# Kernel tuning notes

Measured on AMD Instinct MI355X. Metric: run time of the kernel, lower is better.

## Reference

```python
import jax, jax.numpy as jnp
import numpy as np

N0, N1, N2 = 30000, 90000, 60000          # nodes, edges, triangles
D_IN, D_OUT, HEADS = 256, 128, 4
NNZ0, NNZ1, NNZ2 = 960000, 180000, 180000  # sparse incidence nnz


def setup_inputs() -> dict:
    key = jax.random.key(0)
    ks = jax.random.split(key, 18)
    s = 0.05
    return {
        "x0": jax.random.normal(ks[0], (N0, D_IN), dtype=jnp.float32),
        "x1": jax.random.normal(ks[1], (N1, D_IN), dtype=jnp.float32),
        "x2": jax.random.normal(ks[2], (N2, D_IN), dtype=jnp.float32),
        "rows0": jax.random.randint(ks[3], (NNZ0,), 0, N0),
        "cols0": jax.random.randint(ks[4], (NNZ0,), 0, N0),
        "rows1": jax.random.randint(ks[5], (NNZ1,), 0, N0),
        "cols1": jax.random.randint(ks[6], (NNZ1,), 0, N1),
        "rows2": jax.random.randint(ks[7], (NNZ2,), 0, N0),
        "cols2": jax.random.randint(ks[8], (NNZ2,), 0, N2),
        # per-head parameters (SATLayer_regular), stacked on leading head axis
        "W1": jax.random.normal(ks[9], (HEADS, D_IN, D_OUT), dtype=jnp.float32) * s,
        "b1": jax.random.normal(ks[10], (HEADS, D_OUT), dtype=jnp.float32) * s,
        "a1_w": jax.random.normal(ks[11], (HEADS, D_OUT), dtype=jnp.float32) * s,
        "a1_b": jax.random.normal(ks[12], (HEADS,), dtype=jnp.float32) * s,
        "a2_w": jax.random.normal(ks[13], (HEADS, D_OUT), dtype=jnp.float32) * s,
        "a2_b": jax.random.normal(ks[14], (HEADS,), dtype=jnp.float32) * s,
        "Wagg": jax.random.normal(ks[15], (HEADS, 4 * D_OUT, D_OUT), dtype=jnp.float32) * s,
        "bagg": jax.random.normal(ks[16], (HEADS, D_OUT), dtype=jnp.float32) * s,
    }


def reference(x0, x1, x2, rows0, cols0, rows1, cols1, rows2, cols2,
              W1, b1, a1_w, a1_b, a2_w, a2_b, Wagg, bagg):
    n0 = x0.shape[0]

    def sat_head(W1h, b1h, a1wh, a1bh, a2wh, a2bh, Waggh, baggh):
        # shared Linearlayer1 + ReLU applied to all simplex levels
        xi0 = jax.nn.relu(x0 @ W1h + b1h)   # [n0, d]
        xj1 = jax.nn.relu(x1 @ W1h + b1h)   # [n1, d]
        xj2 = jax.nn.relu(x2 @ W1h + b1h)   # [n2, d]
        a1 = xi0 @ a1wh + a1bh              # [n0] attention source term

        def attention_agg(xj, rows, cols):
            a2 = xj @ a2wh + a2bh                              # [nj]
            att = jax.nn.sigmoid(a1[rows] + a2[cols])          # [nnz]
            msg = att[:, None] * xj[cols]                      # [nnz, d]
            return jax.ops.segment_sum(msg, rows, num_segments=n0)

        agg0 = attention_agg(xi0, rows0, cols0)
        agg1 = attention_agg(xj1, rows1, cols1)
        agg2 = attention_agg(xj2, rows2, cols2)
        cat = jnp.concatenate([xi0, agg0, agg1, agg2], axis=1)  # [n0, 4d]
        return cat @ Waggh + baggh                              # [n0, d]

    # stack over heads, then mean (layer0_1 + torch.mean)
    outs = jax.vmap(sat_head)(W1, b1, a1_w, a1_b, a2_w, a2_b, Wagg, bagg)
    return jnp.mean(outs, axis=0)
```

## Files before the change

kernel.cpp:

```cpp
#include <hip/hip_runtime.h>

typedef __attribute__((ext_vector_type(8))) short short8;
typedef __attribute__((ext_vector_type(4))) float f32x4;
typedef unsigned short ushort_t;
typedef unsigned int uint32;

#define N0 30000
#define N1 90000
#define N2 60000
#define P0 30208
#define S1OFF 30208
#define S2OFF 120320
#define MPAD 180352
#define MT_ALL 1409
#define MT0 236
#define NE0 960000
#define NE1 180000
#define NE2 180000
#define CSTRIDE 30720

__device__ __forceinline__ float bf2f(ushort_t u) {
    union { uint32 i; float f; } v; v.i = ((uint32)u) << 16; return v.f;
}
__device__ __forceinline__ ushort_t f2bf(float f) {
    union { float f; uint32 i; } v; v.f = f;
    uint32 x = v.i;
    x += ((x >> 16) & 1u) + 0x7FFFu;
    return (ushort_t)(x >> 16);
}

__global__ __launch_bounds__(256) void prep_w(const float* __restrict__ W1,
                                              const float* __restrict__ Wagg,
                                              const float* __restrict__ bagg,
                                              ushort_t* __restrict__ W1t,
                                              ushort_t* __restrict__ Wgt,
                                              ushort_t* __restrict__ WgtC,
                                              float* __restrict__ bsum) {
    int idx = blockIdx.x * blockDim.x + threadIdx.x;
    if (idx < 131072) {
        int h = idx >> 15, rem = idx & 32767, n = rem >> 8, k = rem & 255;
        W1t[idx] = f2bf(W1[((size_t)h * 256 + k) * 128 + n]);
    }
    if (idx < 196608) {
        int h = idx / 49152, rem = idx % 49152;
        int l = rem / 16384, rem2 = rem % 16384, n = rem2 >> 7, k = rem2 & 127;
        Wgt[idx] = f2bf(Wagg[((size_t)h * 512 + (l + 1) * 128 + k) * 128 + n]);
    }
    if (idx < 65536) {
        int n = idx >> 9, kk = idx & 511, h = kk >> 7, k = kk & 127;
        WgtC[idx] = f2bf(Wagg[((size_t)h * 512 + k) * 128 + n]);
    }
    if (idx < 128) {
        float s = 0.f;
        #pragma unroll
        for (int h = 0; h < 4; ++h) s += bagg[h * 128 + idx];
        bsum[idx] = s;
    }
}

__global__ __launch_bounds__(256) void csr_zero(int* __restrict__ cur) {
    int i = blockIdx.x * blockDim.x + threadIdx.x;
    if (i < 3 * CSTRIDE) cur[i] = 0;
}

__global__ __launch_bounds__(256) void csr_hist(const int* __restrict__ rows, int nE,
                                                int* __restrict__ cur) {
    int i = blockIdx.x * blockDim.x + threadIdx.x;
    if (i < nE) atomicAdd(cur + rows[i], 1);
}

__global__ __launch_bounds__(1024) void csr_scan(int* __restrict__ curA,
                                                 int* __restrict__ rowPtrA,
                                                 int nE0, int nE1, int nE2) {
    __shared__ int ssum[1024];
    const int b = blockIdx.x;
    int* cur = curA + b * CSTRIDE;
    int* rowPtr = rowPtrA + b * CSTRIDE;
    const int nE = (b == 0) ? nE0 : (b == 1 ? nE1 : nE2);
    const int t = threadIdx.x;
    const int base = t * 30;
    int loc[30];
    int s = 0;
    #pragma unroll
    for (int i = 0; i < 30; ++i) {
        int r = base + i;
        int v = (r < N0) ? cur[r] : 0;
        loc[i] = s; s += v;
    }
    ssum[t] = s;
    __syncthreads();
    for (int off = 1; off < 1024; off <<= 1) {
        int v = (t >= off) ? ssum[t - off] : 0;
        __syncthreads();
        ssum[t] += v;
        __syncthreads();
    }
    int carry = (t == 0) ? 0 : ssum[t - 1];
    #pragma unroll
    for (int i = 0; i < 30; ++i) {
        int r = base + i;
        if (r < N0) {
            int p = carry + loc[i];
            rowPtr[r] = p;
            cur[r] = p;
        }
    }
    if (t == 0) rowPtr[N0] = nE;
}

__global__ __launch_bounds__(256) void csr_scatter(const int* __restrict__ rows,
                                                   const int* __restrict__ cols,
                                                   int nE, int Sl,
                                                   int* __restrict__ cur,
                                                   int* __restrict__ sortedCg) {
    int i = blockIdx.x * blockDim.x + threadIdx.x;
    if (i < nE) {
        int pos = atomicAdd(cur + rows[i], 1);
        sortedCg[pos] = Sl + cols[i];
    }
}

__global__ __launch_bounds__(256) void gemm_x(const float* __restrict__ x0,
                                              const float* __restrict__ x1,
                                              const float* __restrict__ x2,
                                              const ushort_t* __restrict__ W1t,
                                              const float* __restrict__ b1,
                                              ushort_t* __restrict__ Y) {
    __shared__ ushort_t As[128 * 264];
    __shared__ ushort_t Bs[128 * 40];
    const int tid = threadIdx.x;
    const int lane = tid & 63;
    const int wid = tid >> 6;
    const int wm = wid >> 1, wn = wid & 1;
    const int l15 = lane & 15, lg = lane >> 4;
    const int r0 = blockIdx.x * 128;

    const float* src; int jbase, nreal;
    if (r0 < P0)          { src = x0; jbase = r0;         nreal = N0; }
    else if (r0 < S2OFF)  { src = x1; jbase = r0 - S1OFF; nreal = N1; }
    else                  { src = x2; jbase = r0 - S2OFF; nreal = N2; }

    for (int c = 0; c < 32; ++c) {
        int f = tid + c * 256;
        int row = f >> 6, col4 = f & 63;
        int j = jbase + row;
        float vx = 0.f, vy = 0.f, vz = 0.f, vw = 0.f;
        if (j < nreal) {
            const float4 v = *(const float4*)(src + (size_t)j * 256 + col4 * 4);
            vx = v.x; vy = v.y; vz = v.z; vw = v.w;
        }
        ushort_t o[4] __attribute__((aligned(8)));
        o[0] = f2bf(vx); o[1] = f2bf(vy); o[2] = f2bf(vz); o[3] = f2bf(vw);
        *(uint2*)(As + row * 264 + col4 * 4) = *(const uint2*)o;
    }
    __syncthreads();

    for (int h = 0; h < 4; ++h) {
        f32x4 acc[4][4] = {};
        const ushort_t* Bh = W1t + h * 32768;
        for (int kt = 0; kt < 256; kt += 32) {
            #pragma unroll
            for (int u = 0; u < 2; ++u) {
                int g = tid * 2 + u;
                int n = g >> 2, kc = g & 3;
                *(uint4*)(Bs + n * 40 + kc * 8) = *(const uint4*)(Bh + n * 256 + kt + kc * 8);
            }
            __syncthreads();
            short8 af[4], bfr[4];
            #pragma unroll
            for (int m = 0; m < 4; ++m)
                af[m] = *(const short8*)(As + (wm * 64 + m * 16 + l15) * 264 + kt + lg * 8);
            #pragma unroll
            for (int n = 0; n < 4; ++n)
                bfr[n] = *(const short8*)(Bs + (wn * 64 + n * 16 + l15) * 40 + lg * 8);
            #pragma unroll
            for (int m = 0; m < 4; ++m)
                #pragma unroll
                for (int n = 0; n < 4; ++n)
                    acc[m][n] = __builtin_amdgcn_mfma_f32_16x16x32_bf16(af[m], bfr[n], acc[m][n], 0, 0, 0);
            __syncthreads();
        }
        #pragma unroll
        for (int n = 0; n < 4; ++n) {
            int col = wn * 64 + n * 16 + l15;
            float bb = b1[h * 128 + col];
            #pragma unroll
            for (int m = 0; m < 4; ++m)
            #pragma unroll
            for (int j = 0; j < 4; ++j) {
                int row = r0 + wm * 64 + m * 16 + lg * 4 + j;
                float v = acc[m][n][j] + bb;
                v = v > 0.f ? v : 0.f;
                Y[(size_t)row * 512 + h * 128 + col] = f2bf(v);
            }
        }
    }
}

__global__ __launch_bounds__(256)
void gemm_init(const ushort_t* __restrict__ A,
               const ushort_t* __restrict__ B,
               float* __restrict__ outF,
               const float* __restrict__ bias)
{
    __shared__ ushort_t As[128 * 40];
    __shared__ ushort_t Bs[128 * 40];
    const int tid = threadIdx.x;
    const int lane = tid & 63;
    const int wid = tid >> 6;
    const int wm = wid >> 1, wn = wid & 1;
    const int r0 = blockIdx.x * 128;
    const int l15 = lane & 15, lg = lane >> 4;

    f32x4 acc[4][4] = {};

    for (int kt = 0; kt < 512; kt += 32) {
        #pragma unroll
        for (int c = 0; c < 2; ++c) {
            int idx = tid + c * 256;
            int row = idx >> 2, kc = idx & 3;
            uint4 va = *(const uint4*)(A + (size_t)(r0 + row) * 512 + kt + kc * 8);
            *(uint4*)(As + row * 40 + kc * 8) = va;
            uint4 vb = *(const uint4*)(B + (size_t)row * 512 + kt + kc * 8);
            *(uint4*)(Bs + row * 40 + kc * 8) = vb;
        }
        __syncthreads();
        short8 af[4], bfr[4];
        #pragma unroll
        for (int m = 0; m < 4; ++m)
            af[m] = *(const short8*)(As + (wm * 64 + m * 16 + l15) * 40 + lg * 8);
        #pragma unroll
        for (int n = 0; n < 4; ++n)
            bfr[n] = *(const short8*)(Bs + (wn * 64 + n * 16 + l15) * 40 + lg * 8);
        #pragma unroll
        for (int m = 0; m < 4; ++m)
            #pragma unroll
            for (int n = 0; n < 4; ++n)
                acc[m][n] = __builtin_amdgcn_mfma_f32_16x16x32_bf16(af[m], bfr[n], acc[m][n], 0, 0, 0);
        __syncthreads();
    }

    #pragma unroll
    for (int m = 0; m < 4; ++m)
    #pragma unroll
    for (int n = 0; n < 4; ++n)
    #pragma unroll
    for (int j = 0; j < 4; ++j) {
        int row = r0 + wm * 64 + m * 16 + lg * 4 + j;
        int col = wn * 64 + n * 16 + l15;
        if (row < N0) outF[(size_t)row * 128 + col] = 0.25f * (acc[m][n][j] + bias[col]);
    }
}

__global__ __launch_bounds__(256) void gemm_z(const ushort_t* Yin,
                                              const ushort_t* __restrict__ Wgt,
                                              const float* __restrict__ a1w,
                                              const float* __restrict__ a1b,
                                              const float* __restrict__ a2w,
                                              const float* __restrict__ a2b,
                                              float* __restrict__ a1o,
                                              float* __restrict__ a2o,
                                              ushort_t* Yout) {
    __shared__ ushort_t As[128 * 136];
    __shared__ ushort_t Bs[128 * 136];
    __shared__ float a1wS[128], a2wS[128];
    const int tid = threadIdx.x;
    const int h = blockIdx.y;
    const int r0 = blockIdx.x * 128;
    const int l = (r0 < P0) ? 0 : (r0 < S2OFF ? 1 : 2);
    const ushort_t* B = Wgt + ((h * 3 + l) << 14);

    if (tid < 128) {
        a1wS[tid] = a1w[h * 128 + tid];
        a2wS[tid] = a2w[h * 128 + tid];
    }
    #pragma unroll
    for (int c = 0; c < 8; ++c) {
        int idx = tid + c * 256;
        int row = idx >> 4, ch = idx & 15;
        *(uint4*)(As + row * 136 + ch * 8) =
            *(const uint4*)(Yin + (size_t)(r0 + row) * 512 + h * 128 + ch * 8);
        *(uint4*)(Bs + row * 136 + ch * 8) = *(const uint4*)(B + row * 128 + ch * 8);
    }
    __syncthreads();

    {
        int row = tid >> 1, half = tid & 1;
        const ushort_t* yr = As + row * 136 + half * 64;
        float d1 = 0.f, d2 = 0.f;
        #pragma unroll
        for (int t = 0; t < 8; ++t) {
            short8 v = *(const short8*)(yr + t * 8);
            #pragma unroll
            for (int j = 0; j < 8; ++j) {
                float f = bf2f(((const ushort_t*)&v)[j]);
                d2 += f * a2wS[half * 64 + t * 8 + j];
                d1 += f * a1wS[half * 64 + t * 8 + j];
            }
        }
        d2 += __shfl_xor(d2, 1);
        d1 += __shfl_xor(d1, 1);
        if (half == 0) {
            a2o[(size_t)h * MPAD + r0 + row] = d2 + a2b[h];
            if (l == 0) a1o[(size_t)h * P0 + r0 + row] = d1 + a1b[h];
        }
    }

    const int lane = tid & 63;
    const int wid = tid >> 6;
    const int wm = wid >> 1, wn = wid & 1;
    const int l15 = lane & 15, lg = lane >> 4;

    f32x4 acc[4][4] = {};
    #pragma unroll
    for (int kt = 0; kt < 128; kt += 32) {
        short8 af[4], bfr[4];
        #pragma unroll
        for (int m = 0; m < 4; ++m)
            af[m] = *(const short8*)(As + (wm * 64 + m * 16 + l15) * 136 + kt + lg * 8);
        #pragma unroll
        for (int n = 0; n < 4; ++n)
            bfr[n] = *(const short8*)(Bs + (wn * 64 + n * 16 + l15) * 136 + kt + lg * 8);
        #pragma unroll
        for (int m = 0; m < 4; ++m)
            #pragma unroll
            for (int n = 0; n < 4; ++n)
                acc[m][n] = __builtin_amdgcn_mfma_f32_16x16x32_bf16(af[m], bfr[n], acc[m][n], 0, 0, 0);
    }

    #pragma unroll
    for (int m = 0; m < 4; ++m)
    #pragma unroll
    for (int n = 0; n < 4; ++n)
    #pragma unroll
    for (int j = 0; j < 4; ++j) {
        int row = r0 + wm * 64 + m * 16 + lg * 4 + j;
        int col = wn * 64 + n * 16 + l15;
        Yout[(size_t)row * 512 + h * 128 + col] = f2bf(acc[m][n][j]);
    }
}

__global__ __launch_bounds__(256) void pull_agg(const int* __restrict__ rowPtr,
                                                const int* __restrict__ sortedCg,
                                                const float* __restrict__ a1,
                                                const float* __restrict__ a2,
                                                const ushort_t* __restrict__ z,
                                                float* __restrict__ out) {
    int w = blockIdx.x * 4 + (threadIdx.x >> 6);
    if (w >= N0) return;
    const int lane = threadIdx.x & 63;
    const int h = lane >> 4, g = lane & 15;

    const float a1r = a1[(size_t)h * P0 + w];
    const float* a2h = a2 + (size_t)h * MPAD;
    int beg = rowPtr[w], end = rowPtr[w + 1];

    float acc[8] = {0.f, 0.f, 0.f, 0.f, 0.f, 0.f, 0.f, 0.f};
    int e = beg;
    for (; e + 1 < end; e += 2) {
        int cg0 = sortedCg[e], cg1 = sortedCg[e + 1];
        float s0 = a1r + a2h[cg0];
        float s1 = a1r + a2h[cg1];
        float att0 = 0.25f / (1.f + __expf(-s0));
        float att1 = 0.25f / (1.f + __expf(-s1));
        uint4 v0 = *(const uint4*)(z + (size_t)cg0 * 512 + lane * 8);
        uint4 v1 = *(const uint4*)(z + (size_t)cg1 * 512 + lane * 8);
        const ushort_t* u0 = (const ushort_t*)&v0;
        const ushort_t* u1 = (const ushort_t*)&v1;
        #pragma unroll
        for (int j = 0; j < 8; ++j)
            acc[j] += att0 * bf2f(u0[j]) + att1 * bf2f(u1[j]);
    }
    if (e < end) {
        int cg = sortedCg[e];
        float s = a1r + a2h[cg];
        float att = 0.25f / (1.f + __expf(-s));
        uint4 v = *(const uint4*)(z + (size_t)cg * 512 + lane * 8);
        const ushort_t* u = (const ushort_t*)&v;
        #pragma unroll
        for (int j = 0; j < 8; ++j) acc[j] += att * bf2f(u[j]);
    }
    #pragma unroll
    for (int j = 0; j < 8; ++j) {
        acc[j] += __shfl_xor(acc[j], 16);
        acc[j] += __shfl_xor(acc[j], 32);
    }
    float2* p = (float2*)(out + (size_t)w * 128 + g * 8 + h * 2);
    float2 o = *p;
    o.x += acc[h * 2 + 0];
    o.y += acc[h * 2 + 1];
    *p = o;
}

extern "C" void kernel_launch(void* const* d_in, const int* in_sizes, int n_in,
                              void* d_out, int out_size, void* d_ws, size_t ws_size,
                              hipStream_t stream) {
    const float* x0   = (const float*)d_in[0];
    const float* x1   = (const float*)d_in[1];
    const float* x2   = (const float*)d_in[2];
    const int* rows0  = (const int*)d_in[3];
    const int* cols0  = (const int*)d_in[4];
    const int* rows1  = (const int*)d_in[5];
    const int* cols1  = (const int*)d_in[6];
    const int* rows2  = (const int*)d_in[7];
    const int* cols2  = (const int*)d_in[8];
    const float* W1   = (const float*)d_in[9];
    const float* b1   = (const float*)d_in[10];
    const float* a1w  = (const float*)d_in[11];
    const float* a1b  = (const float*)d_in[12];
    const float* a2w  = (const float*)d_in[13];
    const float* a2b  = (const float*)d_in[14];
    const float* Wagg = (const float*)d_in[15];
    const float* bagg = (const float*)d_in[16];
    float* out = (float*)d_out;
    char* ws = (char*)d_ws;

    ushort_t* Y      = (ushort_t*)(ws);
    float*    a1o    = (float*)(ws + 184680448);
    float*    a2o    = (float*)(ws + 185163776);
    ushort_t* W1t    = (ushort_t*)(ws + 188049408);
    ushort_t* Wgt    = (ushort_t*)(ws + 188311552);
    ushort_t* WgtC   = (ushort_t*)(ws + 188704768);
    float*    bsum   = (float*)(ws + 188835840);
    int*      cur    = (int*)(ws + 188836352);
    int*      rowPtr = (int*)(ws + 189204992);
    int*      srtCg  = (int*)(ws + 189573632);

    int* cur0 = cur,              * cur1 = cur + CSTRIDE,    * cur2 = cur + 2 * CSTRIDE;
    int* rp0  = rowPtr,           * rp1  = rowPtr + CSTRIDE, * rp2  = rowPtr + 2 * CSTRIDE;
    int* srt0 = srtCg,            * srt1 = srtCg + NE0,      * srt2 = srtCg + NE0 + NE1;

    csr_zero<<<(3 * CSTRIDE + 255) / 256, 256, 0, stream>>>(cur);
    csr_hist<<<(NE0 + 255) / 256, 256, 0, stream>>>(rows0, NE0, cur0);
    csr_hist<<<(NE1 + 255) / 256, 256, 0, stream>>>(rows1, NE1, cur1);
    csr_hist<<<(NE2 + 255) / 256, 256, 0, stream>>>(rows2, NE2, cur2);
    csr_scan<<<3, 1024, 0, stream>>>(cur, rowPtr, NE0, NE1, NE2);
    csr_scatter<<<(NE0 + 255) / 256, 256, 0, stream>>>(rows0, cols0, NE0, 0,     cur0, srt0);
    csr_scatter<<<(NE1 + 255) / 256, 256, 0, stream>>>(rows1, cols1, NE1, S1OFF, cur1, srt1);
    csr_scatter<<<(NE2 + 255) / 256, 256, 0, stream>>>(rows2, cols2, NE2, S2OFF, cur2, srt2);

    prep_w<<<768, 256, 0, stream>>>(W1, Wagg, bagg, W1t, Wgt, WgtC, bsum);
    gemm_x<<<MT_ALL, 256, 0, stream>>>(x0, x1, x2, W1t, b1, Y);

    gemm_init<<<MT0, 256, 0, stream>>>(Y, WgtC, out, bsum);

    gemm_z<<<dim3(MT_ALL, 4), 256, 0, stream>>>(Y, Wgt, a1w, a1b, a2w, a2b, a1o, a2o, Y);

    pull_agg<<<(N0 + 3) / 4, 256, 0, stream>>>(rp0, srt0, a1o, a2o, Y, out);
    pull_agg<<<(N0 + 3) / 4, 256, 0, stream>>>(rp1, srt1, a1o, a2o, Y, out);
    pull_agg<<<(N0 + 3) / 4, 256, 0, stream>>>(rp2, srt2, a1o, a2o, Y, out);
}
```

Measured before the change: 645.1 us.

## Fuse input GEMM, attention dots, Z projection and init GEMM into one kernel

Merges gemm_x, gemm_init and gemm_z into a single 512-thread kernel. Each head's ReLU(xW1+b) tile stays in swizzled LDS and feeds the attention dot products, the per-level Wagg projection to Z and the level-0 output accumulation directly. This removes the bf16 Y round trip through global memory and two kernel launches. W1/Wgt B-operands are now read straight from global without LDS staging. LDS use rises to 96KB with launch_bounds(512,1), so occupancy is one block per CU.

```diff
diff --git a/kernel.cpp b/kernel.cpp
--- a/kernel.cpp
+++ b/kernel.cpp
@@ -13,7 +13,6 @@
 #define S2OFF 120320
 #define MPAD 180352
 #define MT_ALL 1409
-#define MT0 236
 #define NE0 960000
 #define NE1 180000
 #define NE2 180000
@@ -120,223 +119,197 @@
     }
 }
 
-__global__ __launch_bounds__(256) void gemm_x(const float* __restrict__ x0,
-                                              const float* __restrict__ x1,
-                                              const float* __restrict__ x2,
-                                              const ushort_t* __restrict__ W1t,
-                                              const float* __restrict__ b1,
-                                              ushort_t* __restrict__ Y) {
-    __shared__ ushort_t As[128 * 264];
-    __shared__ ushort_t Bs[128 * 40];
+__global__ __launch_bounds__(512, 1)
+void gemm_fused(const float* __restrict__ x0,
+                const float* __restrict__ x1,
+                const float* __restrict__ x2,
+                const ushort_t* __restrict__ W1t,
+                const float* __restrict__ b1,
+                const ushort_t* __restrict__ Wgt,
+                const ushort_t* __restrict__ WgtC,
+                const float* __restrict__ bsum,
+                const float* __restrict__ a1w, const float* __restrict__ a1b,
+                const float* __restrict__ a2w, const float* __restrict__ a2b,
+                float* __restrict__ a1o, float* __restrict__ a2o,
+                ushort_t* __restrict__ Z, float* __restrict__ outF)
+{
+    __shared__ ushort_t As[128 * 256];
+    __shared__ ushort_t Ys[128 * 128];
     const int tid = threadIdx.x;
     const int lane = tid & 63;
     const int wid = tid >> 6;
-    const int wm = wid >> 1, wn = wid & 1;
+    const int wm = wid >> 2, wn = wid & 3;
     const int l15 = lane & 15, lg = lane >> 4;
     const int r0 = blockIdx.x * 128;
+    const bool isL0 = (r0 < P0);
+    const int l = isL0 ? 0 : (r0 < S2OFF ? 1 : 2);
 
     const float* src; int jbase, nreal;
-    if (r0 < P0)          { src = x0; jbase = r0;         nreal = N0; }
-    else if (r0 < S2OFF)  { src = x1; jbase = r0 - S1OFF; nreal = N1; }
-    else                  { src = x2; jbase = r0 - S2OFF; nreal = N2; }
-
-    for (int c = 0; c < 32; ++c) {
-        int f = tid + c * 256;
-        int row = f >> 6, col4 = f & 63;
+    if (l == 0)      { src = x0; jbase = r0;         nreal = N0; }
+    else if (l == 1) { src = x1; jbase = r0 - S1OFF; nreal = N1; }
+    else             { src = x2; jbase = r0 - S2OFF; nreal = N2; }
+
+    #pragma unroll
+    for (int p = 0; p < 8; ++p) {
+        int chunk = tid + p * 512;
+        int row = chunk >> 5, c = chunk & 31;
         int j = jbase + row;
-        float vx = 0.f, vy = 0.f, vz = 0.f, vw = 0.f;
+        ushort_t o[8] __attribute__((aligned(16)));
         if (j < nreal) {
-            const float4 v = *(const float4*)(src + (size_t)j * 256 + col4 * 4);
-            vx = v.x; vy = v.y; vz = v.z; vw = v.w;
-        }
-        ushort_t o[4] __attribute__((aligned(8)));
-        o[0] = f2bf(vx); o[1] = f2bf(vy); o[2] = f2bf(vz); o[3] = f2bf(vw);
-        *(uint2*)(As + row * 264 + col4 * 4) = *(const uint2*)o;
+            const float4 v0 = *(const float4*)(src + (size_t)j * 256 + c * 8);
+            const float4 v1 = *(const float4*)(src + (size_t)j * 256 + c * 8 + 4);
+            o[0] = f2bf(v0.x); o[1] = f2bf(v0.y); o[2] = f2bf(v0.z); o[3] = f2bf(v0.w);
+            o[4] = f2bf(v1.x); o[5] = f2bf(v1.y); o[6] = f2bf(v1.z); o[7] = f2bf(v1.w);
+        } else {
+            #pragma unroll
+            for (int i = 0; i < 8; ++i) o[i] = 0;
+        }
+        int cs = c ^ (row & 7);
+        *(uint4*)(As + row * 256 + cs * 8) = *(const uint4*)o;
     }
     __syncthreads();
 
+    f32x4 oacc[4][2] = {};
+
     for (int h = 0; h < 4; ++h) {
-        f32x4 acc[4][4] = {};
-        const ushort_t* Bh = W1t + h * 32768;
-        for (int kt = 0; kt < 256; kt += 32) {
-            #pragma unroll
-            for (int u = 0; u < 2; ++u) {
-                int g = tid * 2 + u;
-                int n = g >> 2, kc = g & 3;
-                *(uint4*)(Bs + n * 40 + kc * 8) = *(const uint4*)(Bh + n * 256 + kt + kc * 8);
-            }
-            __syncthreads();
-            short8 af[4], bfr[4];
+        f32x4 acc[4][2] = {};
+        const ushort_t* Bw = W1t + h * 32768;
+        #pragma unroll 2
+        for (int kt = 0; kt < 8; ++kt) {
+            short8 bf[2];
+            #pragma unroll
+            for (int n = 0; n < 2; ++n) {
+                int row = wn * 32 + n * 16 + l15;
+                bf[n] = *(const short8*)(Bw + row * 256 + kt * 32 + lg * 8);
+            }
+            short8 af[4];
+            #pragma unroll
+            for (int m = 0; m < 4; ++m) {
+                int row = wm * 64 + m * 16 + l15;
+                int c = (kt * 4 + lg) ^ (row & 7);
+                af[m] = *(const short8*)(As + row * 256 + c * 8);
+            }
             #pragma unroll
             for (int m = 0; m < 4; ++m)
-                af[m] = *(const short8*)(As + (wm * 64 + m * 16 + l15) * 264 + kt + lg * 8);
-            #pragma unroll
-            for (int n = 0; n < 4; ++n)
-                bfr[n] = *(const short8*)(Bs + (wn * 64 + n * 16 + l15) * 40 + lg * 8);
+                #pragma unroll
+                for (int n = 0; n < 2; ++n)
+                    acc[m][n] = __builtin_amdgcn_mfma_f32_16x16x32_bf16(af[m], bf[n], acc[m][n], 0, 0, 0);
+        }
+        #pragma unroll
+        for (int n = 0; n < 2; ++n) {
+            int col = wn * 32 + n * 16 + l15;
+            float bb = b1[h * 128 + col];
             #pragma unroll
             for (int m = 0; m < 4; ++m)
-                #pragma unroll
-                for (int n = 0; n < 4; ++n)
-                    acc[m][n] = __builtin_amdgcn_mfma_f32_16x16x32_bf16(af[m], bfr[n], acc[m][n], 0, 0, 0);
-            __syncthreads();
-        }
+            #pragma unroll
+            for (int j = 0; j < 4; ++j) {
+                int row = wm * 64 + m * 16 + lg * 4 + j;
+                float v = acc[m][n][j] + bb;
+                v = v > 0.f ? v : 0.f;
+                int cs = (col >> 3) ^ (row & 7);
+                Ys[row * 128 + cs * 8 + (col & 7)] = f2bf(v);
+            }
+        }
+        __syncthreads();
+
+        {
+            int row = tid >> 2, q = tid & 3;
+            float d1 = 0.f, d2 = 0.f;
+            #pragma unroll
+            for (int i = 0; i < 4; ++i) {
+                int c = (q * 4 + i) ^ (row & 7);
+                short8 v = *(const short8*)(Ys + row * 128 + c * 8);
+                #pragma unroll
+                for (int jj = 0; jj < 8; ++jj) {
+                    float f = bf2f(((const ushort_t*)&v)[jj]);
+                    int kk = h * 128 + q * 32 + i * 8 + jj;
+                    d2 += f * a2w[kk];
+                    d1 += f * a1w[kk];
+                }
+            }
+            d1 += __shfl_xor(d1, 1); d1 += __shfl_xor(d1, 2);
+            d2 += __shfl_xor(d2, 1); d2 += __shfl_xor(d2, 2);
+            if (q == 0) {
+                a2o[(size_t)h * MPAD + r0 + row] = d2 + a2b[h];
+                if (isL0) a1o[(size_t)h * P0 + r0 + row] = d1 + a1b[h];
+            }
+        }
+
+        {
+            f32x4 zacc[4][2] = {};
+            const ushort_t* Bz = Wgt + ((h * 3 + l) << 14);
+            #pragma unroll 2
+            for (int kt = 0; kt < 4; ++kt) {
+                short8 bf[2];
+                #pragma unroll
+                for (int n = 0; n < 2; ++n) {
+                    int row = wn * 32 + n * 16 + l15;
+                    bf[n] = *(const short8*)(Bz + row * 128 + kt * 32 + lg * 8);
+                }
+                short8 af[4];
+                #pragma unroll
+                for (int m = 0; m < 4; ++m) {
+                    int row = wm * 64 + m * 16 + l15;
+                    int c = (kt * 4 + lg) ^ (row & 7);
+                    af[m] = *(const short8*)(Ys + row * 128 + c * 8);
+                }
+                #pragma unroll
+                for (int m = 0; m < 4; ++m)
+                    #pragma unroll
+                    for (int n = 0; n < 2; ++n)
+                        zacc[m][n] = __builtin_amdgcn_mfma_f32_16x16x32_bf16(af[m], bf[n], zacc[m][n], 0, 0, 0);
+            }
+            #pragma unroll
+            for (int n = 0; n < 2; ++n)
+            #pragma unroll
+            for (int m = 0; m < 4; ++m)
+            #pragma unroll
+            for (int j = 0; j < 4; ++j) {
+                int row = wm * 64 + m * 16 + lg * 4 + j;
+                int col = wn * 32 + n * 16 + l15;
+                Z[(size_t)(r0 + row) * 512 + h * 128 + col] = f2bf(zacc[m][n][j]);
+            }
+        }
+
+        if (isL0) {
+            #pragma unroll 2
+            for (int kt = 0; kt < 4; ++kt) {
+                short8 bf[2];
+                #pragma unroll
+                for (int n = 0; n < 2; ++n) {
+                    int row = wn * 32 + n * 16 + l15;
+                    bf[n] = *(const short8*)(WgtC + row * 512 + h * 128 + kt * 32 + lg * 8);
+                }
+                short8 af[4];
+                #pragma unroll
+                for (int m = 0; m < 4; ++m) {
+                    int row = wm * 64 + m * 16 + l15;
+                    int c = (kt * 4 + lg) ^ (row & 7);
+                    af[m] = *(const short8*)(Ys + row * 128 + c * 8);
+                }
+                #pragma unroll
+                for (int m = 0; m < 4; ++m)
+                    #pragma unroll
+                    for (int n = 0; n < 2; ++n)
+                        oacc[m][n] = __builtin_amdgcn_mfma_f32_16x16x32_bf16(af[m], bf[n], oacc[m][n], 0, 0, 0);
+            }
+        }
+        __syncthreads();
+    }
+
+    if (isL0) {
         #pragma unroll
-        for (int n = 0; n < 4; ++n) {
-            int col = wn * 64 + n * 16 + l15;
-            float bb = b1[h * 128 + col];
+        for (int n = 0; n < 2; ++n) {
+            int col = wn * 32 + n * 16 + l15;
+            float bs = bsum[col];
             #pragma unroll
             for (int m = 0; m < 4; ++m)
             #pragma unroll
             for (int j = 0; j < 4; ++j) {
                 int row = r0 + wm * 64 + m * 16 + lg * 4 + j;
-                float v = acc[m][n][j] + bb;
-                v = v > 0.f ? v : 0.f;
-                Y[(size_t)row * 512 + h * 128 + col] = f2bf(v);
-            }
-        }
-    }
-}
-
-__global__ __launch_bounds__(256)
-void gemm_init(const ushort_t* __restrict__ A,
-               const ushort_t* __restrict__ B,
-               float* __restrict__ outF,
-               const float* __restrict__ bias)
-{
-    __shared__ ushort_t As[128 * 40];
-    __shared__ ushort_t Bs[128 * 40];
-    const int tid = threadIdx.x;
-    const int lane = tid & 63;
-    const int wid = tid >> 6;
-    const int wm = wid >> 1, wn = wid & 1;
-    const int r0 = blockIdx.x * 128;
-    const int l15 = lane & 15, lg = lane >> 4;
-
-    f32x4 acc[4][4] = {};
-
-    for (int kt = 0; kt < 512; kt += 32) {
-        #pragma unroll
-        for (int c = 0; c < 2; ++c) {
-            int idx = tid + c * 256;
-            int row = idx >> 2, kc = idx & 3;
-            uint4 va = *(const uint4*)(A + (size_t)(r0 + row) * 512 + kt + kc * 8);
-            *(uint4*)(As + row * 40 + kc * 8) = va;
-            uint4 vb = *(const uint4*)(B + (size_t)row * 512 + kt + kc * 8);
-            *(uint4*)(Bs + row * 40 + kc * 8) = vb;
-        }
-        __syncthreads();
-        short8 af[4], bfr[4];
-        #pragma unroll
-        for (int m = 0; m < 4; ++m)
-            af[m] = *(const short8*)(As + (wm * 64 + m * 16 + l15) * 40 + lg * 8);
-        #pragma unroll
-        for (int n = 0; n < 4; ++n)
-            bfr[n] = *(const short8*)(Bs + (wn * 64 + n * 16 + l15) * 40 + lg * 8);
-        #pragma unroll
-        for (int m = 0; m < 4; ++m)
-            #pragma unroll
-            for (int n = 0; n < 4; ++n)
-                acc[m][n] = __builtin_amdgcn_mfma_f32_16x16x32_bf16(af[m], bfr[n], acc[m][n], 0, 0, 0);
-        __syncthreads();
-    }
-
-    #pragma unroll
-    for (int m = 0; m < 4; ++m)
-    #pragma unroll
-    for (int n = 0; n < 4; ++n)
-    #pragma unroll
-    for (int j = 0; j < 4; ++j) {
-        int row = r0 + wm * 64 + m * 16 + lg * 4 + j;
-        int col = wn * 64 + n * 16 + l15;
-        if (row < N0) outF[(size_t)row * 128 + col] = 0.25f * (acc[m][n][j] + bias[col]);
-    }
-}
-
-__global__ __launch_bounds__(256) void gemm_z(const ushort_t* Yin,
-                                              const ushort_t* __restrict__ Wgt,
-                                              const float* __restrict__ a1w,
-                                              const float* __restrict__ a1b,
-                                              const float* __restrict__ a2w,
-                                              const float* __restrict__ a2b,
-                                              float* __restrict__ a1o,
-                                              float* __restrict__ a2o,
-                                              ushort_t* Yout) {
-    __shared__ ushort_t As[128 * 136];
-    __shared__ ushort_t Bs[128 * 136];
-    __shared__ float a1wS[128], a2wS[128];
-    const int tid = threadIdx.x;
-    const int h = blockIdx.y;
-    const int r0 = blockIdx.x * 128;
-    const int l = (r0 < P0) ? 0 : (r0 < S2OFF ? 1 : 2);
-    const ushort_t* B = Wgt + ((h * 3 + l) << 14);
-
-    if (tid < 128) {
-        a1wS[tid] = a1w[h * 128 + tid];
-        a2wS[tid] = a2w[h * 128 + tid];
-    }
-    #pragma unroll
-    for (int c = 0; c < 8; ++c) {
-        int idx = tid + c * 256;
-        int row = idx >> 4, ch = idx & 15;
-        *(uint4*)(As + row * 136 + ch * 8) =
-            *(const uint4*)(Yin + (size_t)(r0 + row) * 512 + h * 128 + ch * 8);
-        *(uint4*)(Bs + row * 136 + ch * 8) = *(const uint4*)(B + row * 128 + ch * 8);
-    }
-    __syncthreads();
-
-    {
-        int row = tid >> 1, half = tid & 1;
-        const ushort_t* yr = As + row * 136 + half * 64;
-        float d1 = 0.f, d2 = 0.f;
-        #pragma unroll
-        for (int t = 0; t < 8; ++t) {
-            short8 v = *(const short8*)(yr + t * 8);
-            #pragma unroll
-            for (int j = 0; j < 8; ++j) {
-                float f = bf2f(((const ushort_t*)&v)[j]);
-                d2 += f * a2wS[half * 64 + t * 8 + j];
-                d1 += f * a1wS[half * 64 + t * 8 + j];
-            }
-        }
-        d2 += __shfl_xor(d2, 1);
-        d1 += __shfl_xor(d1, 1);
-        if (half == 0) {
-            a2o[(size_t)h * MPAD + r0 + row] = d2 + a2b[h];
-            if (l == 0) a1o[(size_t)h * P0 + r0 + row] = d1 + a1b[h];
-        }
-    }
-
-    const int lane = tid & 63;
-    const int wid = tid >> 6;
-    const int wm = wid >> 1, wn = wid & 1;
-    const int l15 = lane & 15, lg = lane >> 4;
-
-    f32x4 acc[4][4] = {};
-    #pragma unroll
-    for (int kt = 0; kt < 128; kt += 32) {
-        short8 af[4], bfr[4];
-        #pragma unroll
-        for (int m = 0; m < 4; ++m)
-            af[m] = *(const short8*)(As + (wm * 64 + m * 16 + l15) * 136 + kt + lg * 8);
-        #pragma unroll
-        for (int n = 0; n < 4; ++n)
-            bfr[n] = *(const short8*)(Bs + (wn * 64 + n * 16 + l15) * 136 + kt + lg * 8);
-        #pragma unroll
-        for (int m = 0; m < 4; ++m)
-            #pragma unroll
-            for (int n = 0; n < 4; ++n)
-                acc[m][n] = __builtin_amdgcn_mfma_f32_16x16x32_bf16(af[m], bfr[n], acc[m][n], 0, 0, 0);
-    }
-
-    #pragma unroll
-    for (int m = 0; m < 4; ++m)
-    #pragma unroll
-    for (int n = 0; n < 4; ++n)
-    #pragma unroll
-    for (int j = 0; j < 4; ++j) {
-        int row = r0 + wm * 64 + m * 16 + lg * 4 + j;
-        int col = wn * 64 + n * 16 + l15;
-        Yout[(size_t)row * 512 + h * 128 + col] = f2bf(acc[m][n][j]);
+                if (row < N0) outF[(size_t)row * 128 + col] = 0.25f * (oacc[m][n][j] + bs);
+            }
+        }
     }
 }
 
@@ -415,7 +388,7 @@
     float* out = (float*)d_out;
     char* ws = (char*)d_ws;
 
-    ushort_t* Y      = (ushort_t*)(ws);
+    ushort_t* Z      = (ushort_t*)(ws);
     float*    a1o    = (float*)(ws + 184680448);
     float*    a2o    = (float*)(ws + 185163776);
     ushort_t* W1t    = (ushort_t*)(ws + 188049408);
@@ -426,9 +399,9 @@
     int*      rowPtr = (int*)(ws + 189204992);
     int*      srtCg  = (int*)(ws + 189573632);
 
-    int* cur0 = cur,              * cur1 = cur + CSTRIDE,    * cur2 = cur + 2 * CSTRIDE;
-    int* rp0  = rowPtr,           * rp1  = rowPtr + CSTRIDE, * rp2  = rowPtr + 2 * CSTRIDE;
-    int* srt0 = srtCg,            * srt1 = srtCg + NE0,      * srt2 = srtCg + NE0 + NE1;
+    int* cur0 = cur,    * cur1 = cur + CSTRIDE,    * cur2 = cur + 2 * CSTRIDE;
+    int* rp0  = rowPtr, * rp1  = rowPtr + CSTRIDE, * rp2  = rowPtr + 2 * CSTRIDE;
+    int* srt0 = srtCg,  * srt1 = srtCg + NE0,      * srt2 = srtCg + NE0 + NE1;
 
     csr_zero<<<(3 * CSTRIDE + 255) / 256, 256, 0, stream>>>(cur);
     csr_hist<<<(NE0 + 255) / 256, 256, 0, stream>>>(rows0, NE0, cur0);
@@ -440,13 +413,10 @@
     csr_scatter<<<(NE2 + 255) / 256, 256, 0, stream>>>(rows2, cols2, NE2, S2OFF, cur2, srt2);
 
     prep_w<<<768, 256, 0, stream>>>(W1, Wagg, bagg, W1t, Wgt, WgtC, bsum);
-    gemm_x<<<MT_ALL, 256, 0, stream>>>(x0, x1, x2, W1t, b1, Y);
-
-    gemm_init<<<MT0, 256, 0, stream>>>(Y, WgtC, out, bsum);
-
-    gemm_z<<<dim3(MT_ALL, 4), 256, 0, stream>>>(Y, Wgt, a1w, a1b, a2w, a2b, a1o, a2o, Y);
-
-    pull_agg<<<(N0 + 3) / 4, 256, 0, stream>>>(rp0, srt0, a1o, a2o, Y, out);
-    pull_agg<<<(N0 + 3) / 4, 256, 0, stream>>>(rp1, srt1, a1o, a2o, Y, out);
-    pull_agg<<<(N0 + 3) / 4, 256, 0, stream>>>(rp2, srt2, a1o, a2o, Y, out);
-}
+    gemm_fused<<<MT_ALL, 512, 0, stream>>>(x0, x1, x2, W1t, b1, Wgt, WgtC, bsum,
+                                           a1w, a1b, a2w, a2b, a1o, a2o, Z, out);
+
+    pull_agg<<<(N0 + 3) / 4, 256, 0, stream>>>(rp0, srt0, a1o, a2o, Z, out);
+    pull_agg<<<(N0 + 3) / 4, 256, 0, stream>>>(rp1, srt1, a1o, a2o, Z, out);
+    pull_agg<<<(N0 + 3) / 4, 256, 0, stream>>>(rp2, srt2, a1o, a2o, Z, out);
+}
```

Result: slower. 724.5 us (+12.3%).

## Split GEMMs into head-parallel tiles, separate attention coefficients, per-level Wagg GEMMs

Applied to the files above, without the earlier changes.

The first projection GEMM now runs as a 2D grid over head-pairs and row tiles, with 512-thread blocks and K-tiled staging. This replaces one block per row tile that looped over all four heads, so there is more parallelism but each x tile is read and converted twice. The attention dot products move into their own kernel. The fused Wagg-projection kernel is replaced by a generic tiled GEMM launched once per simplex level, which adds extra launches and an extra read of Y.

```diff
diff --git a/kernel.cpp b/kernel.cpp
--- a/kernel.cpp
+++ b/kernel.cpp
@@ -12,8 +12,9 @@
 #define S1OFF 30208
 #define S2OFF 120320
 #define MPAD 180352
-#define MT_ALL 1409
 #define MT0 236
+#define MT1 704
+#define MT2 469
 #define NE0 960000
 #define NE1 180000
 #define NE2 180000
@@ -120,79 +121,166 @@
     }
 }
 
-__global__ __launch_bounds__(256) void gemm_x(const float* __restrict__ x0,
-                                              const float* __restrict__ x1,
-                                              const float* __restrict__ x2,
-                                              const ushort_t* __restrict__ W1t,
-                                              const float* __restrict__ b1,
-                                              ushort_t* __restrict__ Y) {
-    __shared__ ushort_t As[128 * 264];
+__global__ __launch_bounds__(512, 4)
+void gemm_y(const float* __restrict__ x0, const float* __restrict__ x1,
+            const float* __restrict__ x2,
+            const ushort_t* __restrict__ W1t, const float* __restrict__ b1,
+            ushort_t* __restrict__ Y)
+{
+    __shared__ ushort_t As[128 * 72];
+    __shared__ ushort_t Bs[2][128 * 72];
+    const int tid = threadIdx.x;
+    const int lane = tid & 63;
+    const int wid = tid >> 6;
+    const int wm = wid >> 2, wn = wid & 3;
+    const int l15 = lane & 15, lg = lane >> 4;
+    const int h0 = blockIdx.x * 2;
+    const int r0 = blockIdx.y * 128;
+
+    const float* src; int jbase, nreal;
+    if (r0 < P0)          { src = x0; jbase = r0;         nreal = N0; }
+    else if (r0 < S2OFF)  { src = x1; jbase = r0 - S1OFF; nreal = N1; }
+    else                  { src = x2; jbase = r0 - S2OFF; nreal = N2; }
+
+    const int srow = tid >> 3, sc8 = tid & 7;
+
+    f32x4 acc[2][4][2] = {};
+
+    for (int kt = 0; kt < 256; kt += 64) {
+        ushort_t oa[2][8] __attribute__((aligned(16)));
+        uint4 breg[2][2];
+        #pragma unroll
+        for (int p = 0; p < 2; ++p) {
+            int row = srow + p * 64;
+            int j = jbase + row;
+            float4 v0 = {}, v1 = {};
+            if (j < nreal) {
+                v0 = *(const float4*)(src + (size_t)j * 256 + kt + sc8 * 8);
+                v1 = *(const float4*)(src + (size_t)j * 256 + kt + sc8 * 8 + 4);
+            }
+            oa[p][0] = f2bf(v0.x); oa[p][1] = f2bf(v0.y);
+            oa[p][2] = f2bf(v0.z); oa[p][3] = f2bf(v0.w);
+            oa[p][4] = f2bf(v1.x); oa[p][5] = f2bf(v1.y);
+            oa[p][6] = f2bf(v1.z); oa[p][7] = f2bf(v1.w);
+            breg[p][0] = *(const uint4*)(W1t + (h0 + 0) * 32768 + row * 256 + kt + sc8 * 8);
+            breg[p][1] = *(const uint4*)(W1t + (h0 + 1) * 32768 + row * 256 + kt + sc8 * 8);
+        }
+
+        __syncthreads();
+        #pragma unroll
+        for (int p = 0; p < 2; ++p) {
+            int row = srow + p * 64;
+            *(uint4*)(As + row * 72 + sc8 * 8) = *(const uint4*)oa[p];
+            *(uint4*)(Bs[0] + row * 72 + sc8 * 8) = breg[p][0];
+            *(uint4*)(Bs[1] + row * 72 + sc8 * 8) = breg[p][1];
+        }
+        __syncthreads();
+
+        #pragma unroll
+        for (int ks = 0; ks < 2; ++ks) {
+            short8 af[4];
+            #pragma unroll
+            for (int m = 0; m < 4; ++m)
+                af[m] = *(const short8*)(As + (wm * 64 + m * 16 + l15) * 72 + ks * 32 + lg * 8);
+            #pragma unroll
+            for (int hh = 0; hh < 2; ++hh) {
+                short8 bf[2];
+                #pragma unroll
+                for (int n = 0; n < 2; ++n)
+                    bf[n] = *(const short8*)(Bs[hh] + (wn * 32 + n * 16 + l15) * 72 + ks * 32 + lg * 8);
+                #pragma unroll
+                for (int m = 0; m < 4; ++m)
+                    #pragma unroll
+                    for (int n = 0; n < 2; ++n)
+                        acc[hh][m][n] = __builtin_amdgcn_mfma_f32_16x16x32_bf16(af[m], bf[n], acc[hh][m][n], 0, 0, 0);
+            }
+        }
+    }
+
+    #pragma unroll
+    for (int hh = 0; hh < 2; ++hh) {
+        int h = h0 + hh;
+        #pragma unroll
+        for (int n = 0; n < 2; ++n) {
+            int col = wn * 32 + n * 16 + l15;
+            float bb = b1[h * 128 + col];
+            #pragma unroll
+            for (int m = 0; m < 4; ++m)
+            #pragma unroll
+            for (int j = 0; j < 4; ++j) {
+                int row = r0 + wm * 64 + m * 16 + lg * 4 + j;
+                float v = acc[hh][m][n][j] + bb;
+                v = v > 0.f ? v : 0.f;
+                Y[(size_t)row * 512 + h * 128 + col] = f2bf(v);
+            }
+        }
+    }
+}
+
+template<int EPI>
+__global__ __launch_bounds__(256)
+void gemm_k(const ushort_t* A, int ldA, int strideA,
+            const ushort_t* __restrict__ B, int K, int strideB,
+            ushort_t* outBF, int outLd, int strideOut,
+            float* __restrict__ outF,
+            const float* __restrict__ bias, int strideBias,
+            int rowGuard)
+{
+    __shared__ ushort_t As[128 * 40];
     __shared__ ushort_t Bs[128 * 40];
     const int tid = threadIdx.x;
     const int lane = tid & 63;
     const int wid = tid >> 6;
     const int wm = wid >> 1, wn = wid & 1;
+    const int r0 = blockIdx.x * 128;
     const int l15 = lane & 15, lg = lane >> 4;
-    const int r0 = blockIdx.x * 128;
-
-    const float* src; int jbase, nreal;
-    if (r0 < P0)          { src = x0; jbase = r0;         nreal = N0; }
-    else if (r0 < S2OFF)  { src = x1; jbase = r0 - S1OFF; nreal = N1; }
-    else                  { src = x2; jbase = r0 - S2OFF; nreal = N2; }
-
-    for (int c = 0; c < 32; ++c) {
-        int f = tid + c * 256;
-        int row = f >> 6, col4 = f & 63;
-        int j = jbase + row;
-        float vx = 0.f, vy = 0.f, vz = 0.f, vw = 0.f;
-        if (j < nreal) {
-            const float4 v = *(const float4*)(src + (size_t)j * 256 + col4 * 4);
-            vx = v.x; vy = v.y; vz = v.z; vw = v.w;
-        }
-        ushort_t o[4] __attribute__((aligned(8)));
-        o[0] = f2bf(vx); o[1] = f2bf(vy); o[2] = f2bf(vz); o[3] = f2bf(vw);
-        *(uint2*)(As + row * 264 + col4 * 4) = *(const uint2*)o;
-    }
-    __syncthreads();
-
-    for (int h = 0; h < 4; ++h) {
-        f32x4 acc[4][4] = {};
-        const ushort_t* Bh = W1t + h * 32768;
-        for (int kt = 0; kt < 256; kt += 32) {
-            #pragma unroll
-            for (int u = 0; u < 2; ++u) {
-                int g = tid * 2 + u;
-                int n = g >> 2, kc = g & 3;
-                *(uint4*)(Bs + n * 40 + kc * 8) = *(const uint4*)(Bh + n * 256 + kt + kc * 8);
-            }
-            __syncthreads();
-            short8 af[4], bfr[4];
-            #pragma unroll
-            for (int m = 0; m < 4; ++m)
-                af[m] = *(const short8*)(As + (wm * 64 + m * 16 + l15) * 264 + kt + lg * 8);
+
+    A += (size_t)blockIdx.y * strideA;
+    B += (size_t)blockIdx.y * strideB;
+    if (outBF) outBF += (size_t)blockIdx.y * strideOut;
+    if (bias) bias += (size_t)blockIdx.y * strideBias;
+
+    f32x4 acc[4][4] = {};
+
+    for (int kt = 0; kt < K; kt += 32) {
+        #pragma unroll
+        for (int c = 0; c < 2; ++c) {
+            int idx = tid + c * 256;
+            int row = idx >> 2, kc = idx & 3;
+            uint4 va = *(const uint4*)(A + (size_t)(r0 + row) * ldA + kt + kc * 8);
+            *(uint4*)(As + row * 40 + kc * 8) = va;
+            uint4 vb = *(const uint4*)(B + (size_t)row * K + kt + kc * 8);
+            *(uint4*)(Bs + row * 40 + kc * 8) = vb;
+        }
+        __syncthreads();
+        short8 af[4], bfr[4];
+        #pragma unroll
+        for (int m = 0; m < 4; ++m)
+            af[m] = *(const short8*)(As + (wm * 64 + m * 16 + l15) * 40 + lg * 8);
+        #pragma unroll
+        for (int n = 0; n < 4; ++n)
+            bfr[n] = *(const short8*)(Bs + (wn * 64 + n * 16 + l15) * 40 + lg * 8);
+        #pragma unroll
+        for (int m = 0; m < 4; ++m)
             #pragma unroll
             for (int n = 0; n < 4; ++n)
-                bfr[n] = *(const short8*)(Bs + (wn * 64 + n * 16 + l15) * 40 + lg * 8);
-            #pragma unroll
-            for (int m = 0; m < 4; ++m)
-                #pragma unroll
-                for (int n = 0; n < 4; ++n)
-                    acc[m][n] = __builtin_amdgcn_mfma_f32_16x16x32_bf16(af[m], bfr[n], acc[m][n], 0, 0, 0);
-            __syncthreads();
-        }
-        #pragma unroll
-        for (int n = 0; n < 4; ++n) {
-            int col = wn * 64 + n * 16 + l15;
-            float bb = b1[h * 128 + col];
-            #pragma unroll
-            for (int m = 0; m < 4; ++m)
-            #pragma unroll
-            for (int j = 0; j < 4; ++j) {
-                int row = r0 + wm * 64 + m * 16 + lg * 4 + j;
-                float v = acc[m][n][j] + bb;
-                v = v > 0.f ? v : 0.f;
-                Y[(size_t)row * 512 + h * 128 + col] = f2bf(v);
-            }
+                acc[m][n] = __builtin_amdgcn_mfma_f32_16x16x32_bf16(af[m], bfr[n], acc[m][n], 0, 0, 0);
+        __syncthreads();
+    }
+
+    #pragma unroll
+    for (int m = 0; m < 4; ++m)
+    #pragma unroll
+    for (int n = 0; n < 4; ++n)
+    #pragma unroll
+    for (int j = 0; j < 4; ++j) {
+        int row = r0 + wm * 64 + m * 16 + lg * 4 + j;
+        int col = wn * 64 + n * 16 + l15;
+        float v = acc[m][n][j];
+        if (EPI == 1) {
+            outBF[(size_t)row * outLd + col] = f2bf(v);
+        } else {
+            if (row < rowGuard) outF[(size_t)row * 128 + col] = 0.25f * (v + bias[col]);
         }
     }
 }
@@ -252,91 +340,34 @@
     }
 }
 
-__global__ __launch_bounds__(256) void gemm_z(const ushort_t* Yin,
-                                              const ushort_t* __restrict__ Wgt,
-                                              const float* __restrict__ a1w,
-                                              const float* __restrict__ a1b,
-                                              const float* __restrict__ a2w,
-                                              const float* __restrict__ a2b,
-                                              float* __restrict__ a1o,
-                                              float* __restrict__ a2o,
-                                              ushort_t* Yout) {
-    __shared__ ushort_t As[128 * 136];
-    __shared__ ushort_t Bs[128 * 136];
-    __shared__ float a1wS[128], a2wS[128];
-    const int tid = threadIdx.x;
-    const int h = blockIdx.y;
-    const int r0 = blockIdx.x * 128;
-    const int l = (r0 < P0) ? 0 : (r0 < S2OFF ? 1 : 2);
-    const ushort_t* B = Wgt + ((h * 3 + l) << 14);
-
-    if (tid < 128) {
-        a1wS[tid] = a1w[h * 128 + tid];
-        a2wS[tid] = a2w[h * 128 + tid];
-    }
-    #pragma unroll
-    for (int c = 0; c < 8; ++c) {
-        int idx = tid + c * 256;
-        int row = idx >> 4, ch = idx & 15;
-        *(uint4*)(As + row * 136 + ch * 8) =
-            *(const uint4*)(Yin + (size_t)(r0 + row) * 512 + h * 128 + ch * 8);
-        *(uint4*)(Bs + row * 136 + ch * 8) = *(const uint4*)(B + row * 128 + ch * 8);
-    }
-    __syncthreads();
-
-    {
-        int row = tid >> 1, half = tid & 1;
-        const ushort_t* yr = As + row * 136 + half * 64;
-        float d1 = 0.f, d2 = 0.f;
-        #pragma unroll
-        for (int t = 0; t < 8; ++t) {
-            short8 v = *(const short8*)(yr + t * 8);
-            #pragma unroll
-            for (int j = 0; j < 8; ++j) {
-                float f = bf2f(((const ushort_t*)&v)[j]);
-                d2 += f * a2wS[half * 64 + t * 8 + j];
-                d1 += f * a1wS[half * 64 + t * 8 + j];
-            }
-        }
-        d2 += __shfl_xor(d2, 1);
-        d1 += __shfl_xor(d1, 1);
-        if (half == 0) {
-            a2o[(size_t)h * MPAD + r0 + row] = d2 + a2b[h];
-            if (l == 0) a1o[(size_t)h * P0 + r0 + row] = d1 + a1b[h];
-        }
-    }
-
-    const int lane = tid & 63;
-    const int wid = tid >> 6;
-    const int wm = wid >> 1, wn = wid & 1;
-    const int l15 = lane & 15, lg = lane >> 4;
-
-    f32x4 acc[4][4] = {};
-    #pragma unroll
-    for (int kt = 0; kt < 128; kt += 32) {
-        short8 af[4], bfr[4];
-        #pragma unroll
-        for (int m = 0; m < 4; ++m)
-            af[m] = *(const short8*)(As + (wm * 64 + m * 16 + l15) * 136 + kt + lg * 8);
-        #pragma unroll
-        for (int n = 0; n < 4; ++n)
-            bfr[n] = *(const short8*)(Bs + (wn * 64 + n * 16 + l15) * 136 + kt + lg * 8);
-        #pragma unroll
-        for (int m = 0; m < 4; ++m)
-            #pragma unroll
-            for (int n = 0; n < 4; ++n)
-                acc[m][n] = __builtin_amdgcn_mfma_f32_16x16x32_bf16(af[m], bfr[n], acc[m][n], 0, 0, 0);
-    }
-
-    #pragma unroll
-    for (int m = 0; m < 4; ++m)
-    #pragma unroll
-    for (int n = 0; n < 4; ++n)
-    #pragma unroll
-    for (int j = 0; j < 4; ++j) {
-        int row = r0 + wm * 64 + m * 16 + lg * 4 + j;
-        int col = wn * 64 + n * 16 + l15;
-        Yout[(size_t)row * 512 + h * 128 + col] = f2bf(acc[m][n][j]);
+__global__ __launch_bounds__(256) void attn_coef(const ushort_t* __restrict__ Y,
+                                                 const float* __restrict__ a1w,
+                                                 const float* __restrict__ a1b,
+                                                 const float* __restrict__ a2w,
+                                                 const float* __restrict__ a2b,
+                                                 float* __restrict__ a1o,
+                                                 float* __restrict__ a2o) {
+    int tid = threadIdx.x, lane = tid & 63, wid = tid >> 6;
+    int R = blockIdx.x * 4 + wid;
+    int h = lane >> 4, s = lane & 15;
+    uint4 v = *(const uint4*)(Y + (size_t)R * 512 + h * 128 + s * 8);
+    const ushort_t* u = (const ushort_t*)&v;
+    float x[8];
+    #pragma unroll
+    for (int i = 0; i < 8; ++i) x[i] = bf2f(u[i]);
+    float d2 = 0.f;
+    #pragma unroll
+    for (int i = 0; i < 8; ++i) d2 += x[i] * a2w[h * 128 + s * 8 + i];
+    #pragma unroll
+    for (int off = 1; off < 16; off <<= 1) d2 += __shfl_xor(d2, off);
+    if (s == 0) a2o[(size_t)h * MPAD + R] = d2 + a2b[h];
+    if (R < N0) {
+        float d1 = 0.f;
+        #pragma unroll
+        for (int i = 0; i < 8; ++i) d1 += x[i] * a1w[h * 128 + s * 8 + i];
+        #pragma unroll
+        for (int off = 1; off < 16; off <<= 1) d1 += __shfl_xor(d1, off);
+        if (s == 0) a1o[(size_t)h * P0 + R] = d1 + a1b[h];
     }
 }
 
@@ -426,9 +457,9 @@
     int*      rowPtr = (int*)(ws + 189204992);
     int*      srtCg  = (int*)(ws + 189573632);
 
-    int* cur0 = cur,              * cur1 = cur + CSTRIDE,    * cur2 = cur + 2 * CSTRIDE;
-    int* rp0  = rowPtr,           * rp1  = rowPtr + CSTRIDE, * rp2  = rowPtr + 2 * CSTRIDE;
-    int* srt0 = srtCg,            * srt1 = srtCg + NE0,      * srt2 = srtCg + NE0 + NE1;
+    int* cur0 = cur,    * cur1 = cur + CSTRIDE,    * cur2 = cur + 2 * CSTRIDE;
+    int* rp0  = rowPtr, * rp1  = rowPtr + CSTRIDE, * rp2  = rowPtr + 2 * CSTRIDE;
+    int* srt0 = srtCg,  * srt1 = srtCg + NE0,      * srt2 = srtCg + NE0 + NE1;
 
     csr_zero<<<(3 * CSTRIDE + 255) / 256, 256, 0, stream>>>(cur);
     csr_hist<<<(NE0 + 255) / 256, 256, 0, stream>>>(rows0, NE0, cur0);
@@ -440,11 +471,19 @@
     csr_scatter<<<(NE2 + 255) / 256, 256, 0, stream>>>(rows2, cols2, NE2, S2OFF, cur2, srt2);
 
     prep_w<<<768, 256, 0, stream>>>(W1, Wagg, bagg, W1t, Wgt, WgtC, bsum);
-    gemm_x<<<MT_ALL, 256, 0, stream>>>(x0, x1, x2, W1t, b1, Y);
-
+    gemm_y<<<dim3(2, 1409), 512, 0, stream>>>(x0, x1, x2, W1t, b1, Y);
+
+    attn_coef<<<MPAD / 4, 256, 0, stream>>>(Y, a1w, a1b, a2w, a2b, a1o, a2o);
     gemm_init<<<MT0, 256, 0, stream>>>(Y, WgtC, out, bsum);
 
-    gemm_z<<<dim3(MT_ALL, 4), 256, 0, stream>>>(Y, Wgt, a1w, a1b, a2w, a2b, a1o, a2o, Y);
+    gemm_k<1><<<dim3(MT0, 4), 256, 0, stream>>>(
+        Y, 512, 128, Wgt + 0 * 16384, 128, 3 * 16384, Y, 512, 128, nullptr, nullptr, 0, 0);
+    gemm_k<1><<<dim3(MT1, 4), 256, 0, stream>>>(
+        Y + (size_t)S1OFF * 512, 512, 128, Wgt + 1 * 16384, 128, 3 * 16384,
+        Y + (size_t)S1OFF * 512, 512, 128, nullptr, nullptr, 0, 0);
+    gemm_k<1><<<dim3(MT2, 4), 256, 0, stream>>>(
+        Y + (size_t)S2OFF * 512, 512, 128, Wgt + 2 * 16384, 128, 3 * 16384,
+        Y + (size_t)S2OFF * 512, 512, 128, nullptr, nullptr, 0, 0);
 
     pull_agg<<<(N0 + 3) / 4, 256, 0, stream>>>(rp0, srt0, a1o, a2o, Y, out);
     pull_agg<<<(N0 + 3) / 4, 256, 0, stream>>>(rp1, srt1, a1o, a2o, Y, out);
```

Measured after the change: 861.7 us. 33.6% more time.
